# Kernel optimization log

Hardware: AMD Instinct MI355X
Metric: run time of the kernel (lower is better)

## Reference

```python
import jax, jax.numpy as jnp
import numpy as np

N_NODES = 50000
N_GRAPHS = 250
NODES_PER_GRAPH = 200
EDGES_PER_GRAPH = 3200  # avg degree 16
F_IN = 128
EMB = 128
HID = 128
VOCAB = 1000
N_REL = 8


def setup_inputs() -> dict:
    key = jax.random.key(0)
    ks = jax.random.split(key, 16)

    # message: col 0 = discrete token id (stored as float), col 1 = continuous value
    disc = jax.random.randint(ks[0], (N_GRAPHS,), 0, VOCAB).astype(jnp.float32)
    cont = jax.random.normal(ks[1], (N_GRAPHS,), dtype=jnp.float32)
    message = jnp.stack([disc, cont], axis=1)  # [B, 2]

    x = jax.random.normal(ks[2], (N_NODES, F_IN), dtype=jnp.float32)

    # within-graph edges: local indices + per-graph node offset
    offs = (jnp.arange(N_GRAPHS, dtype=jnp.int64) * NODES_PER_GRAPH)[:, None]
    src = (jax.random.randint(ks[3], (N_GRAPHS, EDGES_PER_GRAPH), 0, NODES_PER_GRAPH) + offs).reshape(-1)
    dst = (jax.random.randint(ks[4], (N_GRAPHS, EDGES_PER_GRAPH), 0, NODES_PER_GRAPH) + offs).reshape(-1)
    edge_index = jnp.stack([src, dst], axis=0).astype(jnp.int64)  # [2, E]
    edge_type = jax.random.randint(ks[5], (N_GRAPHS * EDGES_PER_GRAPH,), 0, N_REL).astype(jnp.int64)

    batch = jnp.repeat(jnp.arange(N_GRAPHS, dtype=jnp.int64), NODES_PER_GRAPH)  # [N]

    s = 0.05
    W1 = jax.random.normal(ks[6], (N_REL, F_IN, EMB), dtype=jnp.float32) * s
    root1 = jax.random.normal(ks[7], (F_IN, EMB), dtype=jnp.float32) * s
    b1 = jnp.zeros((EMB,), dtype=jnp.float32)
    W2 = jax.random.normal(ks[8], (N_REL, EMB, EMB), dtype=jnp.float32) * s
    root2 = jax.random.normal(ks[9], (EMB, EMB), dtype=jnp.float32) * s
    b2 = jnp.zeros((EMB,), dtype=jnp.float32)
    embed_table = jax.random.normal(ks[10], (VOCAB, EMB), dtype=jnp.float32) * s
    cont_w = jax.random.normal(ks[11], (1, EMB), dtype=jnp.float32) * s
    cont_b = jnp.zeros((EMB,), dtype=jnp.float32)
    msg_w = jax.random.normal(ks[12], (2 * EMB, HID), dtype=jnp.float32) * s
    msg_b = jnp.zeros((HID,), dtype=jnp.float32)

    return {
        "message": message, "x": x, "edge_index": edge_index, "edge_type": edge_type,
        "batch": batch, "max_nodes": NODES_PER_GRAPH,
        "W1": W1, "root1": root1, "b1": b1, "W2": W2, "root2": root2, "b2": b2,
        "embed_table": embed_table, "cont_w": cont_w, "cont_b": cont_b,
        "msg_w": msg_w, "msg_b": msg_b,
    }


def _rgcn_conv(h, src, dst, edge_type, W, root, b, n_nodes, n_rel):
    # per-node per-relation transform, then gather per edge: avoids [E,F,F] weight gather
    hW = jnp.einsum('nf,rfo->nro', h, W)          # [N, R, O]
    msg = hW[src, edge_type]                       # [E, O]
    # mean aggregation per (dst, relation) as in PyG RGCNConv(aggr='mean')
    key_dr = dst * n_rel + edge_type
    cnt = jax.ops.segment_sum(jnp.ones_like(edge_type, dtype=h.dtype), key_dr,
                              num_segments=n_nodes * n_rel)
    norm = 1.0 / jnp.maximum(cnt[key_dr], 1.0)     # [E]
    agg = jax.ops.segment_sum(msg * norm[:, None], dst, num_segments=n_nodes)  # [N, O]
    return agg + h @ root + b


def reference(message, x, edge_index, edge_type, batch, max_nodes,
              W1, root1, b1, W2, root2, b2,
              embed_table, cont_w, cont_b, msg_w, msg_b):
    n_nodes = x.shape[0]
    n_rel = W1.shape[0]
    n_graphs = message.shape[0]
    src, dst = edge_index[0], edge_index[1]

    # --- RGCN node embeddings (2 layers, ReLU between) ---
    h = _rgcn_conv(x, src, dst, edge_type, W1, root1, b1, n_nodes, n_rel)
    h = jax.nn.relu(h)
    node_emb = _rgcn_conv(h, src, dst, edge_type, W2, root2, b2, n_nodes, n_rel)  # [N, EMB]

    # --- message representation ---
    disc_tok = message[:, 0].astype(jnp.int32)
    disc_emb = embed_table[disc_tok]                                   # [B, EMB]
    cont_emb = jax.nn.relu(message[:, 1:2] @ cont_w + cont_b)          # [B, EMB]
    combined = jnp.concatenate([disc_emb, cont_emb], axis=1)           # [B, 2*EMB]
    message_repr = jax.nn.relu(combined @ msg_w + msg_b)               # [B, HID]

    # --- per-node dot score against its graph's message, padded per graph ---
    scores = jnp.einsum('ne,ne->n', node_emb, message_repr[batch])     # [N]
    counts = jax.ops.segment_sum(jnp.ones((n_nodes,), dtype=jnp.int32), batch,
                                 num_segments=n_graphs)
    start = jnp.cumsum(counts) - counts                                # exclusive cumsum
    pos = jnp.arange(n_nodes) - start[batch]                           # slot within graph
    logits = jnp.full((n_graphs, max_nodes), -jnp.inf, dtype=scores.dtype)
    logits = logits.at[batch, pos].set(scores)
    return logits
```

## Files before the change

### kernel.cpp

```cpp
#include <hip/hip_runtime.h>
#include <stdint.h>

#define G_   250
#define P_   200
#define EPG  3200
#define E_   800000
#define F_   128
#define R_   8
#define HROW 136
#define NKEY (R_ * P_)
#define BSET 16384

typedef _Float16 f16x8 __attribute__((ext_vector_type(8)));
typedef _Float16 f16x4 __attribute__((ext_vector_type(4)));
typedef float    f32x16 __attribute__((ext_vector_type(16)));

__global__ __launch_bounds__(256) void k_wstage(const float* __restrict__ W1, const float* __restrict__ root1,
                                                const float* __restrict__ W2, const float* __restrict__ root2,
                                                _Float16* __restrict__ wf) {
  int t = blockIdx.x * 256 + threadIdx.x;
  int n = t & 127;
  int k = (t >> 7) & 127;
  int rl_ = t >> 14;
  int r = rl_ % 9, l = rl_ / 9;
  const float* Wl = (l == 0) ? W1 : W2;
  const float* rt = (l == 0) ? root1 : root2;
  float v = (r < 8) ? Wl[(r * F_ + k) * F_ + n] : rt[k * F_ + n];
  int lane = (n & 31) | (((k >> 3) & 1) << 5);
  int j = k & 7, kt = k >> 4, ntj = n >> 5;
  wf[(l * 9 + r) * BSET + ((kt * 4 + ntj) * 64 + lane) * 8 + j] = (_Float16)v;
}

__global__ __launch_bounds__(1024) __attribute__((amdgpu_waves_per_eu(4, 4))) void k_main(
    const float* __restrict__ x, const int* __restrict__ ei, const int* __restrict__ et,
    const _Float16* __restrict__ wf, const float* __restrict__ b1, const float* __restrict__ b2,
    const float* __restrict__ message, const float* __restrict__ embed,
    const float* __restrict__ cw, const float* __restrict__ cb,
    const float* __restrict__ mw, const float* __restrict__ mb,
    float* __restrict__ out) {
  __shared__ __attribute__((aligned(16))) _Float16 hbuf[P_ * HROW];
  __shared__ __attribute__((aligned(16))) _Float16 Bstage[2][BSET];
  __shared__ unsigned short csrS[EPG];
  __shared__ int offsS[NKEY + 1];
  __shared__ float msgS[F_ + 1];
  __shared__ float scoreS[2 * P_];

  int g = blockIdx.x, tid = threadIdx.x;
  int lane = tid & 63, wave = tid >> 6;
  int m32 = lane & 31, kh = lane >> 5;

  f16x8 stA = *((const f16x8*)(wf + tid * 8));
  f16x8 stB = *((const f16x8*)(wf + 8192 + tid * 8));

  int*   Sint = (int*)Bstage[1];
  int*   cnt  = Sint;
  int*   cur  = Sint + 1600;
  int*   eRec = Sint + 3200;
  float* comb = (float*)(Sint + 6400);
  float* red  = (float*)(Sint + 6656);

  for (int i = tid; i < P_ * 32; i += 1024) {
    int row = i >> 5, c4 = i & 31;
    const float4 v = ((const float4*)x)[(g * P_ + row) * 32 + c4];
    f16x4 pk = { (_Float16)v.x, (_Float16)v.y, (_Float16)v.z, (_Float16)v.w };
    *((f16x4*)&hbuf[row * HROW + c4 * 4]) = pk;
  }
  for (int i = tid; i < NKEY; i += 1024) { cnt[i] = 0; cur[i] = 0; }
  if (tid < F_) {
    int tok = (int)message[g * 2];
    float cont = message[g * 2 + 1];
    comb[tid] = embed[tok * F_ + tid];
    float ce = cont * cw[tid] + cb[tid];
    comb[F_ + tid] = ce > 0.0f ? ce : 0.0f;
  }
  __syncthreads();

  int base = g * EPG, nbase = g * P_;
  if (wave < 12) {
    for (int e = wave * 64 + lane; e < EPG; e += 768) {
      int s = ei[base + e] - nbase;
      int d = ei[E_ + base + e] - nbase;
      int r = et[base + e];
      eRec[e] = s | (d << 8) | (r << 16);
      atomicAdd(&cnt[r * P_ + d], 1);
    }
  } else {
    int t2 = tid - 768;
    int col = t2 & 127, seg = t2 >> 7;
    float acc = 0.0f;
#pragma unroll 16
    for (int k2 = seg * 128; k2 < seg * 128 + 128; k2++) acc += comb[k2] * mw[k2 * F_ + col];
    red[t2] = acc;
  }
  __syncthreads();

  if (wave == 0) {
    int4 vv[8];
    int osum = 0;
    if (lane < 50) {
      const int4* cp = (const int4*)(cnt + lane * 32);
#pragma unroll
      for (int i = 0; i < 8; i++) { vv[i] = cp[i]; osum += vv[i].x + vv[i].y + vv[i].z + vv[i].w; }
    }
    int incl = osum;
#pragma unroll
    for (int d = 1; d < 64; d <<= 1) {
      int t2 = __shfl_up(incl, d, 64);
      if (lane >= d) incl += t2;
    }
    int run = incl - osum;
    if (lane < 50) {
#pragma unroll
      for (int i = 0; i < 8; i++) {
        offsS[lane * 32 + i * 4 + 0] = run; run += vv[i].x;
        offsS[lane * 32 + i * 4 + 1] = run; run += vv[i].y;
        offsS[lane * 32 + i * 4 + 2] = run; run += vv[i].z;
        offsS[lane * 32 + i * 4 + 3] = run; run += vv[i].w;
      }
    }
    if (lane == 0) offsS[NKEY] = EPG;
  } else if (wave == 1) {
    float m0 = mb[lane] + red[lane] + red[128 + lane];
    float m1 = mb[lane + 64] + red[lane + 64] + red[192 + lane];
    m0 = m0 > 0.0f ? m0 : 0.0f;
    m1 = m1 > 0.0f ? m1 : 0.0f;
    msgS[lane] = m0; msgS[lane + 64] = m1;
    float p = m0 * b2[lane] + m1 * b2[lane + 64];
#pragma unroll
    for (int d = 32; d > 0; d >>= 1) p += __shfl_xor(p, d, 64);
    if (lane == 0) msgS[F_] = p;
  }
  __syncthreads();

  for (int e = tid; e < EPG; e += 1024) {
    int rec = eRec[e];
    int s = rec & 255, d = (rec >> 8) & 255, r = rec >> 16;
    int key = r * P_ + d;
    int pos = atomicAdd(&cur[key], 1);
    csrS[offsS[key] + pos] = (unsigned short)s;
  }
  *((f16x8*)(&Bstage[0][tid * 8])) = stA;
  *((f16x8*)(&Bstage[0][8192 + tid * 8])) = stB;
  __syncthreads();

  int jobId = wave;
  bool act = jobId < 14;
  int mt = jobId >> 1, nh = jobId & 1;
  int rowM = mt * 32 + m32;
  int ck = kh * 8;
  float db2 = msgS[F_];

  f32x16 acc0, acc1;
#pragma unroll
  for (int i = 0; i < 16; i++) { acc0[i] = 0.0f; acc1[i] = 0.0f; }

  for (int it = 0; it < 18; it++) {
    f16x8 nA, nB;
    if (it < 17) {
      const _Float16* wn = wf + (it + 1) * BSET;
      nA = *((const f16x8*)(wn + tid * 8));
      nB = *((const f16x8*)(wn + 8192 + tid * 8));
    }
    int r = it - (it >= 9 ? 9 : 0);
    const _Float16* Bb = Bstage[it & 1];
    if (act) {
      f16x8 a[8];
      if (r < 8) {
        int o = 0, n = 0;
        if (rowM < P_) { int key = r * P_ + rowM; o = offsS[key]; n = offsS[key + 1] - o; }
        f16x8 z = {0, 0, 0, 0, 0, 0, 0, 0};
#pragma unroll
        for (int kt = 0; kt < 8; kt++) a[kt] = z;
        for (int t = 0; t < n; t++) {
          int sc = (int)csrS[o + t];
          const _Float16* hp = &hbuf[sc * HROW + ck];
#pragma unroll
          for (int kt = 0; kt < 8; kt++) a[kt] += *((const f16x8*)(hp + kt * 16));
        }
        float nf = (n > 0) ? 1.0f / (float)n : 0.0f;
        _Float16 nh16 = (_Float16)nf;
#pragma unroll
        for (int kt = 0; kt < 8; kt++) a[kt] *= nh16;
      } else {
        int rA = rowM < P_ ? rowM : P_ - 1;
        const _Float16* hp = &hbuf[rA * HROW + ck];
#pragma unroll
        for (int kt = 0; kt < 8; kt++) a[kt] = *((const f16x8*)(hp + kt * 16));
      }
#pragma unroll
      for (int kt = 0; kt < 8; kt++) {
        f16x8 b0 = *((const f16x8*)&Bb[((kt * 4 + nh * 2 + 0) * 64 + lane) * 8]);
        acc0 = __builtin_amdgcn_mfma_f32_32x32x16_f16(a[kt], b0, acc0, 0, 0, 0);
        f16x8 b1v = *((const f16x8*)&Bb[((kt * 4 + nh * 2 + 1) * 64 + lane) * 8]);
        acc1 = __builtin_amdgcn_mfma_f32_32x32x16_f16(a[kt], b1v, acc1, 0, 0, 0);
      }
    }
    if (it < 17) {
      _Float16* Bw = Bstage[(it + 1) & 1];
      *((f16x8*)(&Bw[tid * 8])) = nA;
      *((f16x8*)(&Bw[8192 + tid * 8])) = nB;
    }
    __syncthreads();
    if (it == 8) {
      if (act) {
#pragma unroll
        for (int nt2 = 0; nt2 < 2; nt2++) {
          int col = (nh * 2 + nt2) * 32 + m32;
          float bias = b1[col];
          const f32x16& ac = nt2 ? acc1 : acc0;
#pragma unroll
          for (int reg = 0; reg < 16; reg++) {
            int row = mt * 32 + (reg & 3) + 8 * (reg >> 2) + 4 * kh;
            if (row < P_) {
              float v = ac[reg] + bias;
              v = v > 0.0f ? v : 0.0f;
              hbuf[row * HROW + col] = (_Float16)v;
            }
          }
        }
      }
      __syncthreads();
#pragma unroll
      for (int i = 0; i < 16; i++) { acc0[i] = 0.0f; acc1[i] = 0.0f; }
    }
  }

  if (act) {
#pragma unroll
    for (int reg = 0; reg < 16; reg++) {
      int row = mt * 32 + (reg & 3) + 8 * (reg >> 2) + 4 * kh;
      float p = acc0[reg] * msgS[(nh * 2 + 0) * 32 + m32]
              + acc1[reg] * msgS[(nh * 2 + 1) * 32 + m32];
      p += __shfl_xor(p, 16, 32);
      p += __shfl_xor(p, 8, 32);
      p += __shfl_xor(p, 4, 32);
      p += __shfl_xor(p, 2, 32);
      p += __shfl_xor(p, 1, 32);
      if (m32 == 0 && row < P_) scoreS[nh * P_ + row] = p;
    }
  }
  __syncthreads();
  for (int i = tid; i < P_; i += 1024)
    out[g * P_ + i] = scoreS[i] + scoreS[P_ + i] + db2;
}

extern "C" void kernel_launch(void* const* d_in, const int* in_sizes, int n_in,
                              void* d_out, int out_size, void* d_ws, size_t ws_size,
                              hipStream_t stream) {
  const float* message = (const float*)d_in[0];
  const float* x       = (const float*)d_in[1];
  const int*   ei      = (const int*)d_in[2];
  const int*   et      = (const int*)d_in[3];
  const float* W1      = (const float*)d_in[6];
  const float* root1   = (const float*)d_in[7];
  const float* b1      = (const float*)d_in[8];
  const float* W2      = (const float*)d_in[9];
  const float* root2   = (const float*)d_in[10];
  const float* b2      = (const float*)d_in[11];
  const float* embed   = (const float*)d_in[12];
  const float* cw      = (const float*)d_in[13];
  const float* cb      = (const float*)d_in[14];
  const float* mw      = (const float*)d_in[15];
  const float* mb      = (const float*)d_in[16];

  _Float16* wfrag = (_Float16*)d_ws;
  float*    out   = (float*)d_out;

  hipLaunchKernelGGL(k_wstage, dim3(1152), dim3(256), 0, stream, W1, root1, W2, root2, wfrag);
  hipLaunchKernelGGL(k_main, dim3(G_), dim3(1024), 0, stream, x, ei, et, wfrag, b1, b2,
                     message, embed, cw, cb, mw, mb, out);
}
```

Baseline: 181.6 us.

## Split K dimension across wave pairs instead of N halves in RGCN aggregation

Each wave pair now splits the 128-wide feature (K) dimension in half rather than splitting output columns, so each wave gathers only 64 features per neighbor and computes all four N tiles. This halves the redundant neighbor gather work per wave, which previously re-read full rows in both N-half waves. The partial accumulators are reduced through shared memory with extra barriers, and the next CSR index is prefetched in the gather loop. It adds register pressure (four accumulators) and eight extra syncthreads per layer.

```diff
diff --git a/kernel.cpp b/kernel.cpp
--- a/kernel.cpp
+++ b/kernel.cpp
@@ -43,7 +43,6 @@
   __shared__ unsigned short csrS[EPG];
   __shared__ int offsS[NKEY + 1];
   __shared__ float msgS[F_ + 1];
-  __shared__ float scoreS[2 * P_];
 
   int g = blockIdx.x, tid = threadIdx.x;
   int lane = tid & 63, wave = tid >> 6;
@@ -145,14 +144,16 @@
 
   int jobId = wave;
   bool act = jobId < 14;
-  int mt = jobId >> 1, nh = jobId & 1;
+  int mt = jobId >> 1, kth = jobId & 1;
   int rowM = mt * 32 + m32;
-  int ck = kh * 8;
+  int ck = kth * 64 + kh * 8;
   float db2 = msgS[F_];
 
-  f32x16 acc0, acc1;
-#pragma unroll
-  for (int i = 0; i < 16; i++) { acc0[i] = 0.0f; acc1[i] = 0.0f; }
+  f32x16 acc[4];
+#pragma unroll
+  for (int nt = 0; nt < 4; nt++)
+#pragma unroll
+    for (int i = 0; i < 16; i++) acc[nt][i] = 0.0f;
 
   for (int it = 0; it < 18; it++) {
     f16x8 nA, nB;
@@ -164,35 +165,38 @@
     int r = it - (it >= 9 ? 9 : 0);
     const _Float16* Bb = Bstage[it & 1];
     if (act) {
-      f16x8 a[8];
+      f16x8 a[4];
       if (r < 8) {
         int o = 0, n = 0;
         if (rowM < P_) { int key = r * P_ + rowM; o = offsS[key]; n = offsS[key + 1] - o; }
         f16x8 z = {0, 0, 0, 0, 0, 0, 0, 0};
 #pragma unroll
-        for (int kt = 0; kt < 8; kt++) a[kt] = z;
+        for (int kt = 0; kt < 4; kt++) a[kt] = z;
+        int sNext = (n > 0) ? (int)csrS[o] : 0;
         for (int t = 0; t < n; t++) {
-          int sc = (int)csrS[o + t];
+          int sc = sNext;
+          if (t + 1 < n) sNext = (int)csrS[o + t + 1];
           const _Float16* hp = &hbuf[sc * HROW + ck];
 #pragma unroll
-          for (int kt = 0; kt < 8; kt++) a[kt] += *((const f16x8*)(hp + kt * 16));
+          for (int kt = 0; kt < 4; kt++) a[kt] += *((const f16x8*)(hp + kt * 16));
         }
         float nf = (n > 0) ? 1.0f / (float)n : 0.0f;
         _Float16 nh16 = (_Float16)nf;
 #pragma unroll
-        for (int kt = 0; kt < 8; kt++) a[kt] *= nh16;
+        for (int kt = 0; kt < 4; kt++) a[kt] *= nh16;
       } else {
         int rA = rowM < P_ ? rowM : P_ - 1;
         const _Float16* hp = &hbuf[rA * HROW + ck];
 #pragma unroll
-        for (int kt = 0; kt < 8; kt++) a[kt] = *((const f16x8*)(hp + kt * 16));
-      }
-#pragma unroll
-      for (int kt = 0; kt < 8; kt++) {
-        f16x8 b0 = *((const f16x8*)&Bb[((kt * 4 + nh * 2 + 0) * 64 + lane) * 8]);
-        acc0 = __builtin_amdgcn_mfma_f32_32x32x16_f16(a[kt], b0, acc0, 0, 0, 0);
-        f16x8 b1v = *((const f16x8*)&Bb[((kt * 4 + nh * 2 + 1) * 64 + lane) * 8]);
-        acc1 = __builtin_amdgcn_mfma_f32_32x32x16_f16(a[kt], b1v, acc1, 0, 0, 0);
+        for (int kt = 0; kt < 4; kt++) a[kt] = *((const f16x8*)(hp + kt * 16));
+      }
+#pragma unroll
+      for (int kt = 0; kt < 4; kt++) {
+#pragma unroll
+        for (int nt = 0; nt < 4; nt++) {
+          f16x8 b = *((const f16x8*)&Bb[(((kth * 4 + kt) * 4 + nt) * 64 + lane) * 8]);
+          acc[nt] = __builtin_amdgcn_mfma_f32_32x32x16_f16(a[kt], b, acc[nt], 0, 0, 0);
+        }
       }
     }
     if (it < 17) {
@@ -202,17 +206,32 @@
     }
     __syncthreads();
     if (it == 8) {
-      if (act) {
-#pragma unroll
-        for (int nt2 = 0; nt2 < 2; nt2++) {
-          int col = (nh * 2 + nt2) * 32 + m32;
+      float* Xbuf = (float*)Bstage[0];
+#pragma unroll
+      for (int nt = 0; nt < 4; nt++) {
+        if (act && kth == 1) {
+#pragma unroll
+          for (int reg = 0; reg < 16; reg++)
+            Xbuf[mt * 1024 + reg * 64 + lane] = acc[nt][reg];
+        }
+        __syncthreads();
+        if (act && kth == 0) {
+#pragma unroll
+          for (int reg = 0; reg < 16; reg++)
+            acc[nt][reg] += Xbuf[mt * 1024 + reg * 64 + lane];
+        }
+        __syncthreads();
+      }
+      if (act && kth == 0) {
+#pragma unroll
+        for (int nt = 0; nt < 4; nt++) {
+          int col = nt * 32 + m32;
           float bias = b1[col];
-          const f32x16& ac = nt2 ? acc1 : acc0;
 #pragma unroll
           for (int reg = 0; reg < 16; reg++) {
             int row = mt * 32 + (reg & 3) + 8 * (reg >> 2) + 4 * kh;
             if (row < P_) {
-              float v = ac[reg] + bias;
+              float v = acc[nt][reg] + bias;
               v = v > 0.0f ? v : 0.0f;
               hbuf[row * HROW + col] = (_Float16)v;
             }
@@ -221,27 +240,46 @@
       }
       __syncthreads();
 #pragma unroll
-      for (int i = 0; i < 16; i++) { acc0[i] = 0.0f; acc1[i] = 0.0f; }
-    }
-  }
-
-  if (act) {
-#pragma unroll
-    for (int reg = 0; reg < 16; reg++) {
-      int row = mt * 32 + (reg & 3) + 8 * (reg >> 2) + 4 * kh;
-      float p = acc0[reg] * msgS[(nh * 2 + 0) * 32 + m32]
-              + acc1[reg] * msgS[(nh * 2 + 1) * 32 + m32];
-      p += __shfl_xor(p, 16, 32);
-      p += __shfl_xor(p, 8, 32);
-      p += __shfl_xor(p, 4, 32);
-      p += __shfl_xor(p, 2, 32);
-      p += __shfl_xor(p, 1, 32);
-      if (m32 == 0 && row < P_) scoreS[nh * P_ + row] = p;
-    }
-  }
-  __syncthreads();
-  for (int i = tid; i < P_; i += 1024)
-    out[g * P_ + i] = scoreS[i] + scoreS[P_ + i] + db2;
+      for (int nt = 0; nt < 4; nt++)
+#pragma unroll
+        for (int i = 0; i < 16; i++) acc[nt][i] = 0.0f;
+    }
+  }
+
+  {
+    float* Xbuf = (float*)Bstage[0];
+#pragma unroll
+    for (int nt = 0; nt < 4; nt++) {
+      if (act && kth == 1) {
+#pragma unroll
+        for (int reg = 0; reg < 16; reg++)
+          Xbuf[mt * 1024 + reg * 64 + lane] = acc[nt][reg];
+      }
+      __syncthreads();
+      if (act && kth == 0) {
+#pragma unroll
+        for (int reg = 0; reg < 16; reg++)
+          acc[nt][reg] += Xbuf[mt * 1024 + reg * 64 + lane];
+      }
+      __syncthreads();
+    }
+    if (act && kth == 0) {
+#pragma unroll
+      for (int reg = 0; reg < 16; reg++) {
+        int row = mt * 32 + (reg & 3) + 8 * (reg >> 2) + 4 * kh;
+        float p = 0.0f;
+#pragma unroll
+        for (int nt = 0; nt < 4; nt++)
+          p += acc[nt][reg] * msgS[nt * 32 + m32];
+        p += __shfl_xor(p, 16, 32);
+        p += __shfl_xor(p, 8, 32);
+        p += __shfl_xor(p, 4, 32);
+        p += __shfl_xor(p, 2, 32);
+        p += __shfl_xor(p, 1, 32);
+        if (m32 == 0 && row < P_) out[g * P_ + row] = p + db2;
+      }
+    }
+  }
 }
 
 extern "C" void kernel_launch(void* const* d_in, const int* in_sizes, int n_in,
```

After: 242.7 us. 33.6% more time.
